# Kernel optimization log

Hardware: AMD Instinct MI355X
Metric: run time of the kernel (lower is better)

The kernel has to match this reference:

```python
import jax, jax.numpy as jnp
import numpy as np
from jax import lax

K = 9          # box kernel side
PAD = K // 2   # same padding
K_SUM = float(K * K * K)


def _box_sum(x):
    """Sliding-window sum over a 9x9x9 box, zero-padded (separable 1D convs).
    x: [B, 1, D, H, W] -> same shape."""
    dn = ('NCDHW', 'OIDHW', 'NCDHW')
    for ax in range(3):  # D, H, W
        kshape = [1, 1, 1, 1, 1]
        kshape[2 + ax] = K
        w = jnp.ones(kshape, dtype=x.dtype)
        pad = [(0, 0), (0, 0), (0, 0)]
        pad[ax] = (PAD, PAD)
        x = lax.conv_general_dilated(x, w, window_strides=(1, 1, 1),
                                     padding=pad, dimension_numbers=dn)
    return x


def setup_inputs() -> dict:
    key = jax.random.key(0)
    k1, k2 = jax.random.split(key)
    shape = (2, 1, 192, 192, 192)  # [B, 1, D, H, W]
    I = jax.random.uniform(k1, shape, dtype=jnp.float32)
    J = jax.random.uniform(k2, shape, dtype=jnp.float32)
    return {"I": I, "J": J}


def reference(I, J):
    II = I * I
    JJ = J * J
    IJ = I * J
    I_sum = _box_sum(I)
    J_sum = _box_sum(J)
    II_sum = _box_sum(II)
    JJ_sum = _box_sum(JJ)
    IJ_sum = _box_sum(IJ)
    I_u = I / K_SUM
    J_u = J / K_SUM
    cross = IJ_sum - I_sum * J_u - J_sum * I_u + I_u * J_u * K_SUM
    I_var = II_sum - 2 * I_sum * I_u + I_u * I_u * K_SUM
    J_var = JJ_sum - 2 * J_sum * J_u + J_u * J_u * K_SUM
    top = cross * cross
    bottom = I_var * J_var + 1e-5
    return -jnp.mean(top / bottom)
```

## Files before the change

### kernel.cpp

```cpp
#include <hip/hip_runtime.h>
#include <hip/hip_bf16.h>

#define WDIM 192
#define PLANE (192 * 192)
#define VOL (192 * 192 * 192)
#define HC 24
#define TR (HC + 8)
#define ROWW 200
#define DC 24

__global__ void zero_out_k(float* out) { out[0] = 0.0f; }

static __device__ inline unsigned int pk_bf16(float a, float b) {
    union { __hip_bfloat162 v; unsigned int u; } cvt;
    cvt.v = __float22bfloat162_rn(make_float2(a, b));
    return cvt.u;
}
static __device__ inline float bf_lo(unsigned int u) {
    union { unsigned int u; float f; } c; c.u = u << 16; return c.f;
}
static __device__ inline float bf_hi(unsigned int u) {
    union { unsigned int u; float f; } c; c.u = u & 0xffff0000u; return c.f;
}

__global__ __launch_bounds__(192) void wh_pass(const float* __restrict__ I,
                                               const float* __restrict__ J,
                                               uint4* __restrict__ B) {
    __shared__ unsigned int sPK[TR * ROWW];
    const int t = threadIdx.x;
    const int d = blockIdx.x >> 3;
    const int c = blockIdx.x & 7;
    const int h0 = c * HC;

    const size_t dbase = (size_t)d * PLANE;

    {
        const int i0 = t;
        if (i0 < 256) {
            const int row = i0 >> 3;
            const int p = i0 & 7;
            const int col = (p < 4) ? p : (192 + p);
            sPK[row * ROWW + col] = 0u;
        }
        const int i1 = t + 192;
        if (i1 < 256) {
            const int row = i1 >> 3;
            const int p = i1 & 7;
            const int col = (p < 4) ? p : (192 + p);
            sPK[row * ROWW + col] = 0u;
        }
    }

    #pragma unroll
    for (int i = 0; i < 8; ++i) {
        const int idx4 = i * 192 + t;
        const int row  = idx4 / 48;
        const int col4 = (idx4 - row * 48) * 4;
        const int h = h0 - 4 + row;
        float4 vI = make_float4(0.f, 0.f, 0.f, 0.f);
        float4 vJ = vI;
        if (h >= 0 && h < WDIM) {
            vI = *(const float4*)(I + dbase + (size_t)h * WDIM + col4);
            vJ = *(const float4*)(J + dbase + (size_t)h * WDIM + col4);
        }
        uint4 u;
        u.x = pk_bf16(vI.x, vJ.x);
        u.y = pk_bf16(vI.y, vJ.y);
        u.z = pk_bf16(vI.z, vJ.z);
        u.w = pk_bf16(vI.w, vJ.w);
        *(uint4*)&sPK[row * ROWW + 4 + col4] = u;
    }
    __syncthreads();

    float ring0[9], ring1[9], ring2[9], ring3[9], ring4[9];
    #pragma unroll
    for (int j = 0; j < 9; ++j) { ring0[j]=0.f; ring1[j]=0.f; ring2[j]=0.f; ring3[j]=0.f; ring4[j]=0.f; }
    float s0 = 0.f, s1 = 0.f, s2 = 0.f, s3 = 0.f, s4 = 0.f;

    unsigned int uA[9], uB[9];
    #pragma unroll
    for (int k = 0; k < 9; ++k) uA[k] = sPK[0 * ROWW + t + k];

    #pragma unroll
    for (int s = 0; s < TR; ++s) {
        if (s + 1 < TR) {
            if ((s & 1) == 0) {
                #pragma unroll
                for (int k = 0; k < 9; ++k) uB[k] = sPK[(s + 1) * ROWW + t + k];
            } else {
                #pragma unroll
                for (int k = 0; k < 9; ++k) uA[k] = sPK[(s + 1) * ROWW + t + k];
            }
        }
        float w0 = 0.f, w1 = 0.f, w2 = 0.f, w3 = 0.f, w4 = 0.f;
        #pragma unroll
        for (int k = 0; k < 9; ++k) {
            const unsigned int u = ((s & 1) == 0) ? uA[k] : uB[k];
            const float a = bf_lo(u);
            const float b = bf_hi(u);
            w0 += a; w1 += b;
            w2 += a * a; w3 += b * b; w4 += a * b;
        }
        const int j = s % 9;
        s0 += w0 - ring0[j]; ring0[j] = w0;
        s1 += w1 - ring1[j]; ring1[j] = w1;
        s2 += w2 - ring2[j]; ring2[j] = w2;
        s3 += w3 - ring3[j]; ring3[j] = w3;
        s4 += w4 - ring4[j]; ring4[j] = w4;

        if (s >= 8) {
            const int h_out = h0 + s - 8;
            const unsigned int cu = sPK[(s - 4) * ROWW + t + 4];
            const float ci = bf_lo(cu);
            const float cj = bf_hi(cu);
            uint4 q;
            q.x = pk_bf16(s0, s1);
            q.y = pk_bf16(s2, s3);
            q.z = pk_bf16(s4, ci);
            q.w = pk_bf16(cj, 0.f);
            B[dbase + (size_t)h_out * WDIM + t] = q;
        }
    }
}

__global__ __launch_bounds__(192) void d_pass(const uint4* __restrict__ B,
                                              float* __restrict__ out) {
    const int t = threadIdx.x;
    const int h = blockIdx.x >> 3;
    const int c = blockIdx.x & 7;
    const int d0 = c * DC;
    const int base_h = h * WDIM + t;

    float r0[9], r1[9], r2[9], r3[9], r4[9], rI[9], rJ[9];
    #pragma unroll
    for (int j = 0; j < 9; ++j) { r0[j]=0.f; r1[j]=0.f; r2[j]=0.f; r3[j]=0.f; r4[j]=0.f; rI[j]=0.f; rJ[j]=0.f; }
    float s0 = 0.f, s1 = 0.f, s2 = 0.f, s3 = 0.f, s4 = 0.f;

    const float inv_k = 1.0f / 729.0f;
    float local = 0.f;

    uint4 qA[8], qB[8];
    #pragma unroll
    for (int i = 0; i < 8; ++i) {
        const int d_in = d0 - 4 + i;
        qA[i] = make_uint4(0u, 0u, 0u, 0u);
        if (d_in >= 0 && d_in < WDIM)
            qA[i] = B[(size_t)d_in * PLANE + base_h];
    }

    #pragma unroll
    for (int g = 0; g < 4; ++g) {
        if (g + 1 < 4) {
            #pragma unroll
            for (int i = 0; i < 8; ++i) {
                const int s = (g + 1) * 8 + i;
                const int d_in = d0 - 4 + s;
                uint4 v = make_uint4(0u, 0u, 0u, 0u);
                if (d_in >= 0 && d_in < WDIM)
                    v = B[(size_t)d_in * PLANE + base_h];
                if ((g & 1) == 0) qB[i] = v; else qA[i] = v;
            }
        }
        #pragma unroll
        for (int i = 0; i < 8; ++i) {
            const int s = g * 8 + i;
            const uint4 q = ((g & 1) == 0) ? qA[i] : qB[i];
            const float f0 = bf_lo(q.x), f1 = bf_hi(q.x);
            const float f2 = bf_lo(q.y), f3 = bf_hi(q.y);
            const float f4 = bf_lo(q.z), f5 = bf_hi(q.z);
            const float f6 = bf_lo(q.w);
            const int j = s % 9;
            s0 += f0 - r0[j]; r0[j] = f0;
            s1 += f1 - r1[j]; r1[j] = f1;
            s2 += f2 - r2[j]; r2[j] = f2;
            s3 += f3 - r3[j]; r3[j] = f3;
            s4 += f4 - r4[j]; r4[j] = f4;
            rI[j] = f5; rJ[j] = f6;

            if (s >= 8) {
                const int jc = (s - 4) % 9;
                const float vi = rI[jc];
                const float vj = rJ[jc];
                const float Iu = vi * inv_k;
                const float Ju = vj * inv_k;
                const float cross = s4 - s0 * Ju - s1 * Iu + Iu * Ju * 729.0f;
                const float Ivar  = s2 - 2.0f * s0 * Iu + Iu * Iu * 729.0f;
                const float Jvar  = s3 - 2.0f * s1 * Ju + Ju * Ju * 729.0f;
                local += (cross * cross) / (Ivar * Jvar + 1e-5f);
            }
        }
    }

    __shared__ float sred[192];
    sred[t] = local;
    __syncthreads();
    if (t < 64) {
        float v = sred[t] + sred[t + 64] + sred[t + 128];
        #pragma unroll
        for (int off = 32; off; off >>= 1) v += __shfl_down(v, off);
        if (t == 0) {
            atomicAdd(out, v * (-1.0f / 14155776.0f));
        }
    }
}

extern "C" void kernel_launch(void* const* d_in, const int* in_sizes, int n_in,
                              void* d_out, int out_size, void* d_ws, size_t ws_size,
                              hipStream_t stream) {
    const float* I = (const float*)d_in[0];
    const float* J = (const float*)d_in[1];
    float* out = (float*)d_out;

    uint4* B = (uint4*)d_ws;

    zero_out_k<<<1, 1, 0, stream>>>(out);

    for (int b = 0; b < 2; ++b) {
        const float* Ib = I + (size_t)b * VOL;
        const float* Jb = J + (size_t)b * VOL;
        wh_pass<<<192 * 8, 192, 0, stream>>>(Ib, Jb, B);
        d_pass<<<192 * 8, 192, 0, stream>>>(B, out);
    }
}
```

Measured before the change: 264.4 us.

## Shrink intermediate to 12 bytes and batch both volumes in one launch

The WH pass now writes a 12-byte packed record (five bf16 box sums) instead of 16 bytes, dropping the center I/J values. The D pass reads those center values in full fp32 precision directly from the original inputs. Both batches run in one launch each via blockIdx.y when the workspace is large enough, halving the launch count and filling the GPU more. The cost is extra fp32 global reads in the D pass and unaligned 12-byte accesses that may split into narrower loads.

After: 246.3 us. 1.07x faster.

```diff
diff --git a/kernel.cpp b/kernel.cpp
--- a/kernel.cpp
+++ b/kernel.cpp
@@ -25,30 +25,32 @@
 
 __global__ __launch_bounds__(192) void wh_pass(const float* __restrict__ I,
                                                const float* __restrict__ J,
-                                               uint4* __restrict__ B) {
+                                               unsigned int* __restrict__ B) {
     __shared__ unsigned int sPK[TR * ROWW];
     const int t = threadIdx.x;
     const int d = blockIdx.x >> 3;
     const int c = blockIdx.x & 7;
     const int h0 = c * HC;
 
+    const size_t bofs = (size_t)blockIdx.y * VOL;
+    const float* Ib = I + bofs;
+    const float* Jb = J + bofs;
+    unsigned int* Bb = B + bofs * 3;
+
     const size_t dbase = (size_t)d * PLANE;
 
     {
-        const int i0 = t;
-        if (i0 < 256) {
-            const int row = i0 >> 3;
-            const int p = i0 & 7;
-            const int col = (p < 4) ? p : (192 + p);
-            sPK[row * ROWW + col] = 0u;
-        }
-        const int i1 = t + 192;
-        if (i1 < 256) {
+        if (t < 256 - 192) {
+            const int i1 = t + 192;
             const int row = i1 >> 3;
             const int p = i1 & 7;
             const int col = (p < 4) ? p : (192 + p);
             sPK[row * ROWW + col] = 0u;
         }
+        const int row = t >> 3;
+        const int p = t & 7;
+        const int col = (p < 4) ? p : (192 + p);
+        if (t < 256) sPK[row * ROWW + col] = 0u;
     }
 
     #pragma unroll
@@ -60,8 +62,8 @@
         float4 vI = make_float4(0.f, 0.f, 0.f, 0.f);
         float4 vJ = vI;
         if (h >= 0 && h < WDIM) {
-            vI = *(const float4*)(I + dbase + (size_t)h * WDIM + col4);
-            vJ = *(const float4*)(J + dbase + (size_t)h * WDIM + col4);
+            vI = *(const float4*)(Ib + dbase + (size_t)h * WDIM + col4);
+            vJ = *(const float4*)(Jb + dbase + (size_t)h * WDIM + col4);
         }
         uint4 u;
         u.x = pk_bf16(vI.x, vJ.x);
@@ -110,20 +112,19 @@
 
         if (s >= 8) {
             const int h_out = h0 + s - 8;
-            const unsigned int cu = sPK[(s - 4) * ROWW + t + 4];
-            const float ci = bf_lo(cu);
-            const float cj = bf_hi(cu);
-            uint4 q;
+            const size_t idx = dbase + (size_t)h_out * WDIM + t;
+            uint3 q;
             q.x = pk_bf16(s0, s1);
             q.y = pk_bf16(s2, s3);
-            q.z = pk_bf16(s4, ci);
-            q.w = pk_bf16(cj, 0.f);
-            B[dbase + (size_t)h_out * WDIM + t] = q;
-        }
-    }
-}
-
-__global__ __launch_bounds__(192) void d_pass(const uint4* __restrict__ B,
+            q.z = pk_bf16(s4, 0.f);
+            *(uint3*)(Bb + idx * 3) = q;
+        }
+    }
+}
+
+__global__ __launch_bounds__(192) void d_pass(const unsigned int* __restrict__ B,
+                                              const float* __restrict__ I,
+                                              const float* __restrict__ J,
                                               float* __restrict__ out) {
     const int t = threadIdx.x;
     const int h = blockIdx.x >> 3;
@@ -131,21 +132,28 @@
     const int d0 = c * DC;
     const int base_h = h * WDIM + t;
 
-    float r0[9], r1[9], r2[9], r3[9], r4[9], rI[9], rJ[9];
-    #pragma unroll
-    for (int j = 0; j < 9; ++j) { r0[j]=0.f; r1[j]=0.f; r2[j]=0.f; r3[j]=0.f; r4[j]=0.f; rI[j]=0.f; rJ[j]=0.f; }
+    const size_t bofs = (size_t)blockIdx.y * VOL;
+    const float* Ib = I + bofs;
+    const float* Jb = J + bofs;
+    const unsigned int* Bb = B + bofs * 3;
+
+    float r0[9], r1[9], r2[9], r3[9], r4[9];
+    #pragma unroll
+    for (int j = 0; j < 9; ++j) { r0[j]=0.f; r1[j]=0.f; r2[j]=0.f; r3[j]=0.f; r4[j]=0.f; }
     float s0 = 0.f, s1 = 0.f, s2 = 0.f, s3 = 0.f, s4 = 0.f;
 
     const float inv_k = 1.0f / 729.0f;
     float local = 0.f;
 
-    uint4 qA[8], qB[8];
+    uint3 qA[8], qB[8];
+    float2 cA[8], cB[8];
     #pragma unroll
     for (int i = 0; i < 8; ++i) {
         const int d_in = d0 - 4 + i;
-        qA[i] = make_uint4(0u, 0u, 0u, 0u);
+        qA[i] = make_uint3(0u, 0u, 0u);
         if (d_in >= 0 && d_in < WDIM)
-            qA[i] = B[(size_t)d_in * PLANE + base_h];
+            qA[i] = *(const uint3*)(Bb + ((size_t)d_in * PLANE + base_h) * 3);
+        cA[i] = make_float2(0.f, 0.f);
     }
 
     #pragma unroll
@@ -155,34 +163,35 @@
             for (int i = 0; i < 8; ++i) {
                 const int s = (g + 1) * 8 + i;
                 const int d_in = d0 - 4 + s;
-                uint4 v = make_uint4(0u, 0u, 0u, 0u);
+                uint3 v = make_uint3(0u, 0u, 0u);
                 if (d_in >= 0 && d_in < WDIM)
-                    v = B[(size_t)d_in * PLANE + base_h];
-                if ((g & 1) == 0) qB[i] = v; else qA[i] = v;
+                    v = *(const uint3*)(Bb + ((size_t)d_in * PLANE + base_h) * 3);
+                const int d_out = d0 + s - 8;
+                const size_t cidx = (size_t)d_out * PLANE + base_h;
+                const float ci = Ib[cidx];
+                const float cj = Jb[cidx];
+                if ((g & 1) == 0) { qB[i] = v; cB[i] = make_float2(ci, cj); }
+                else              { qA[i] = v; cA[i] = make_float2(ci, cj); }
             }
         }
         #pragma unroll
         for (int i = 0; i < 8; ++i) {
             const int s = g * 8 + i;
-            const uint4 q = ((g & 1) == 0) ? qA[i] : qB[i];
+            const uint3 q = ((g & 1) == 0) ? qA[i] : qB[i];
             const float f0 = bf_lo(q.x), f1 = bf_hi(q.x);
             const float f2 = bf_lo(q.y), f3 = bf_hi(q.y);
-            const float f4 = bf_lo(q.z), f5 = bf_hi(q.z);
-            const float f6 = bf_lo(q.w);
+            const float f4 = bf_lo(q.z);
             const int j = s % 9;
             s0 += f0 - r0[j]; r0[j] = f0;
             s1 += f1 - r1[j]; r1[j] = f1;
             s2 += f2 - r2[j]; r2[j] = f2;
             s3 += f3 - r3[j]; r3[j] = f3;
             s4 += f4 - r4[j]; r4[j] = f4;
-            rI[j] = f5; rJ[j] = f6;
 
             if (s >= 8) {
-                const int jc = (s - 4) % 9;
-                const float vi = rI[jc];
-                const float vj = rJ[jc];
-                const float Iu = vi * inv_k;
-                const float Ju = vj * inv_k;
+                const float2 cc = ((g & 1) == 0) ? cA[i] : cB[i];
+                const float Iu = cc.x * inv_k;
+                const float Ju = cc.y * inv_k;
                 const float cross = s4 - s0 * Ju - s1 * Iu + Iu * Ju * 729.0f;
                 const float Ivar  = s2 - 2.0f * s0 * Iu + Iu * Iu * 729.0f;
                 const float Jvar  = s3 - 2.0f * s1 * Ju + Ju * Ju * 729.0f;
@@ -210,15 +219,20 @@
     const float* I = (const float*)d_in[0];
     const float* J = (const float*)d_in[1];
     float* out = (float*)d_out;
-
-    uint4* B = (uint4*)d_ws;
+    unsigned int* B = (unsigned int*)d_ws;
 
     zero_out_k<<<1, 1, 0, stream>>>(out);
 
-    for (int b = 0; b < 2; ++b) {
-        const float* Ib = I + (size_t)b * VOL;
-        const float* Jb = J + (size_t)b * VOL;
-        wh_pass<<<192 * 8, 192, 0, stream>>>(Ib, Jb, B);
-        d_pass<<<192 * 8, 192, 0, stream>>>(B, out);
-    }
-}
+    const size_t need2 = (size_t)2 * VOL * 12;
+    if (ws_size >= need2) {
+        wh_pass<<<dim3(1536, 2), 192, 0, stream>>>(I, J, B);
+        d_pass <<<dim3(1536, 2), 192, 0, stream>>>(B, I, J, out);
+    } else {
+        for (int b = 0; b < 2; ++b) {
+            const float* Ib = I + (size_t)b * VOL;
+            const float* Jb = J + (size_t)b * VOL;
+            wh_pass<<<dim3(1536, 1), 192, 0, stream>>>(Ib, Jb, B);
+            d_pass <<<dim3(1536, 1), 192, 0, stream>>>(B, Ib, Jb, out);
+        }
+    }
+}
```
